# Performance work log

Measured on AMD Instinct MI355X. Metric: run time of the kernel, lower is better.

## Reference

```python
import jax, jax.numpy as jnp
import numpy as np

B, T, NIN, H, DMAX, K = 32, 128, 64, 512, 50, 4
D = DMAX + 1
TAU, THR, VRESET, REF_STEPS, DT, BETA = 10.0, 1.0, 0.0, 2, 1.0, 4.0


def setup_inputs() -> dict:
    key = jax.random.key(0)
    k0, k1, k2, k3 = jax.random.split(key, 4)
    spike_input = (jax.random.uniform(k0, (B, T, NIN)) < 0.05).astype(jnp.float32)
    w_ih = jax.random.normal(k1, (H, NIN)) * (1.0 / np.sqrt(NIN))
    delay_raw_ih = jax.random.normal(k2, (H, NIN))
    w_read = jax.random.normal(k3, (H,)) * (1.0 / np.sqrt(H))
    b_read = jnp.zeros((), jnp.float32)
    win = T // K
    mask = np.zeros((K, T), np.float32)
    for k in range(K):
        mask[k, k * win + 8:(k + 1) * win] = 1.0
    return {"spike_input": spike_input, "w_ih": w_ih, "delay_raw_ih": delay_raw_ih,
            "w_read": w_read, "b_read": b_read, "slot_mask": jnp.asarray(mask)}


@jax.custom_vjp
def spike_fn(x):
    return (x >= 0).astype(x.dtype)

def _sf_fwd(x):
    return spike_fn(x), x

def _sf_bwd(x, g):
    s = jax.nn.sigmoid(BETA * x)
    return (g * BETA * s * (1 - s),)

spike_fn.defvjp(_sf_fwd, _sf_bwd)


def reference(spike_input, w_ih, delay_raw_ih, w_read, b_read, slot_mask):
    # fractional per-synapse delays in [0, DMAX]
    d = jax.nn.sigmoid(delay_raw_ih) * DMAX        # [H, NIN]
    d0 = jnp.floor(d)
    frac = d - d0                                   # [H, NIN]
    i0 = d0.astype(jnp.int32)
    i1 = jnp.minimum(i0 + 1, DMAX)

    def gather(buf_t, idx):
        # buf_t [B, NIN, D], idx [H, NIN] -> [B, H, NIN]
        return jnp.take_along_axis(buf_t[:, None, :, :], idx[None, :, :, None], axis=-1)[..., 0]

    def step(carry, x_t):
        v, ref, buf, tot, fired = carry
        buf_t = jnp.swapaxes(buf, 1, 2)             # [B, NIN, D]
        delayed = gather(buf_t, i0) * (1 - frac) + gather(buf_t, i1) * frac  # [B,H,NIN]
        I = jnp.einsum('bhi,hi->bh', delayed, w_ih)
        not_ref = ref <= 0
        v_new = jnp.where(not_ref, v + (DT / TAU) * (-(v - VRESET) + I), v)
        spk = spike_fn(v_new - THR) * not_ref.astype(v.dtype)
        v_post = v_new * (1 - spk) + VRESET * spk
        ref_new = jnp.where(spk > 0, REF_STEPS, jnp.maximum(ref - 1, 0))
        # shift delay buffer: newest input at slot 0 (read happens BEFORE insert, as in source)
        buf_new = jnp.concatenate([x_t[:, None, :], buf[:, :-1, :]], axis=1)
        return (v_post, ref_new, buf_new, tot + spk.sum(1), jnp.maximum(fired, spk)), spk

    carry0 = (jnp.full((B, H), VRESET, jnp.float32),
              jnp.zeros((B, H), jnp.int32),
              jnp.zeros((B, D, NIN), jnp.float32),
              jnp.zeros((B,), jnp.float32),
              jnp.zeros((B, H), jnp.float32))
    xs = jnp.swapaxes(spike_input, 0, 1)            # [T, B, NIN]
    (_, _, _, total_h_spk, fired), spikes = jax.lax.scan(step, carry0, xs)
    # slot-windowed spike accumulation + linear readout
    acc = jnp.einsum('kt,tbh->bkh', slot_mask, spikes)
    logits = jnp.einsum('bkh,h->bk', acc, w_read) + b_read
    return logits
```

## Files before the change

### kernel.cpp

```cpp
#include <hip/hip_runtime.h>

#define NB 32
#define NT 128
#define NI 64
#define NH 512
#define HGB 32
#define PSTR 45
typedef unsigned long long u64;
typedef unsigned int u32;
typedef unsigned char u8;

#define OFF_P 0
#define OFF_BUF 23040
#define OFF_WL 23040
#define OFF_KL (23040 + 33280)
#define OFF_RL (OFF_KL + 2048)
#define OFF_MM (OFF_RL + 2048)
#define SMEM_BYTES (OFF_MM + 1024)

__global__ __launch_bounds__(1024, 4) void cur_kernel(
    const float* __restrict__ x, const float* __restrict__ w_ih,
    const float* __restrict__ draw, float4* __restrict__ Ig) {
  __shared__ char smem[SMEM_BYTES];
  u64* P = (u64*)(smem + OFF_P);
  float* xl = (float*)(smem + OFF_BUF);
  float4* Wl4 = (float4*)(smem + OFF_WL);
  u32* Klw = (u32*)(smem + OFF_KL);
  u32* Rlw = (u32*)(smem + OFF_RL);
  u64* Mm = (u64*)(smem + OFF_MM);

  const int tid = threadIdx.x;
  const int lane = tid & 63;
  const int wv = tid >> 6;
  const int hl = lane & 31;
  const int ch = lane >> 5;
  const int c = wv * 2 + ch;
  const int b = blockIdx.x;
  const int hg = blockIdx.y;

  {
    const float* xb = x + (size_t)b * (NT * NI);
    #pragma unroll
    for (int k2 = 0; k2 < 2; ++k2) {
      int e = (k2 * 1024 + tid) * 4;
      float4 v = *(const float4*)(xb + e);
      float* row = xl + (e >> 6) * (NI + 1) + (e & 63);
      row[0] = v.x; row[1] = v.y; row[2] = v.z; row[3] = v.w;
    }
  }
  __syncthreads();

  #pragma unroll
  for (int j = 0; j < 8; ++j) {
    int idx = wv * 8 + j;
    int i = idx >> 1;
    int h2 = idx & 1;
    u64 m = __ballot(xl[(h2 * 64 + lane) * (NI + 1) + i] != 0.0f);
    if (lane == 0) Mm[i * 2 + h2] = m;
  }
  __syncthreads();

  for (int idx = tid; idx < NI * PSTR; idx += 1024) {
    int i = idx / PSTR;
    int k = idx - i * PSTR;
    u64 m0 = Mm[i * 2], m1 = Mm[i * 2 + 1];
    u32 lo = 0, hi = 0;
    if (k >= 13) {
      int t = (k - 13) * 4;
      u32 nib = (u32)(((t < 64) ? (m0 >> t) : (m1 >> (t - 64))) & 15);
      lo = (nib * 0x00204081u) & 0x01010101u;
    }
    if (k + 1 >= 13 && k + 1 < 45) {
      int t = (k - 12) * 4;
      u32 nib = (u32)(((t < 64) ? (m0 >> t) : (m1 >> (t - 64))) & 15);
      hi = (nib * 0x00204081u) & 0x01010101u;
    }
    P[idx] = ((u64)hi << 32) | lo;
  }

  if (tid < 512) {
    int i4 = tid & 15, hh = tid >> 4;
    int h = hg * HGB + hh;
    float4 wv4 = *((const float4*)(w_ih + (size_t)h * NI) + i4);
    float4 rv4 = *((const float4*)(draw + (size_t)h * NI) + i4);
    float wa[4] = {wv4.x, wv4.y, wv4.z, wv4.w};
    float ra[4] = {rv4.x, rv4.y, rv4.z, rv4.w};
    float w0s[4], w1s[4];
    u32 kword = 0, rword = 0;
    #pragma unroll
    for (int jj = 0; jj < 4; ++jj) {
      float sig = 1.0f / (1.0f + expf(-ra[jj]));
      float d = sig * 50.0f;
      float d0f = floorf(d);
      float frac = d - d0f;
      int i0 = (int)d0f;
      float w0 = wa[jj] * (1.0f - frac);
      float w1 = wa[jj] * frac;
      if (i0 >= 50) { w0 += w1; w1 = 0.0f; i0 = 50; }
      w0s[jj] = w0; w1s[jj] = w1;
      int q = 50 - i0;
      kword |= (u32)(q >> 2) << (8 * jj);
      rword |= (u32)((q & 3) << 3) << (8 * jj);
    }
    Wl4[(2 * i4) * HGB + hh]     = make_float4(w0s[0], w1s[0], w0s[1], w1s[1]);
    Wl4[(2 * i4 + 1) * HGB + hh] = make_float4(w0s[2], w1s[2], w0s[3], w1s[3]);
    Klw[i4 * HGB + hh] = kword;
    Rlw[i4 * HGB + hh] = rword;
  }
  __syncthreads();

  float acc[4];
  #pragma unroll
  for (int j = 0; j < 4; ++j) acc[j] = 0.0f;

  u32 kall[16], rall[16];
  #pragma unroll
  for (int q = 0; q < 16; ++q) {
    kall[q] = Klw[q * HGB + hl];
    rall[q] = Rlw[q * HGB + hl];
  }
  const u64* Pc = P + c;

#define TAPS(IDX, W0, W1, KO, R8)                              \
  do {                                                         \
    u64 A = Pc[(IDX) * PSTR + (KO)];                           \
    u64 s1 = A >> (R8);                                        \
    u32 a0 = (u32)s1, a1 = (u32)(s1 >> 32);                    \
    float f0 = (float)(a0 & 255u);                             \
    float f1 = (float)((a0 >> 8) & 255u);                      \
    float f2 = (float)((a0 >> 16) & 255u);                     \
    float f3 = (float)(a0 >> 24);                              \
    float f4 = (float)(a1 & 255u);                             \
    acc[0] += (W0) * f1 + (W1) * f0;                           \
    acc[1] += (W0) * f2 + (W1) * f1;                           \
    acc[2] += (W0) * f3 + (W1) * f2;                           \
    acc[3] += (W0) * f4 + (W1) * f3;                           \
  } while (0)

  #pragma unroll
  for (int i4 = 0; i4 < 16; ++i4) {
    u32 kw = kall[i4];
    u32 rw = rall[i4];
    float4 wa = Wl4[(2 * i4) * HGB + hl];
    float4 wb = Wl4[(2 * i4 + 1) * HGB + hl];
    TAPS(4 * i4 + 0, wa.x, wa.y, (kw & 255u), (rw & 255u));
    TAPS(4 * i4 + 1, wa.z, wa.w, ((kw >> 8) & 255u), ((rw >> 8) & 255u));
    TAPS(4 * i4 + 2, wb.x, wb.y, ((kw >> 16) & 255u), ((rw >> 16) & 255u));
    TAPS(4 * i4 + 3, wb.z, wb.w, (kw >> 24), (rw >> 24));
    __builtin_amdgcn_sched_group_barrier(0x100, 2, 0);
    __builtin_amdgcn_sched_group_barrier(0x002, 26, 0);
    __builtin_amdgcn_sched_group_barrier(0x100, 2, 0);
    __builtin_amdgcn_sched_group_barrier(0x002, 26, 0);
    __builtin_amdgcn_sched_group_barrier(0x100, 2, 0);
    __builtin_amdgcn_sched_group_barrier(0x002, 26, 0);
  }
#undef TAPS

  Ig[((size_t)b * NH + hg * HGB + hl) * (NT / 4) + c] =
      make_float4(acc[0], acc[1], acc[2], acc[3]);
}

__global__ __launch_bounds__(512) void lifred_kernel(
    const float4* __restrict__ Ig, const float* __restrict__ w_read,
    const float* __restrict__ b_read, float* __restrict__ out) {
  const int b = blockIdx.x;
  const int tid = threadIdx.x;
  const float4* row = Ig + ((size_t)b * NH + tid) * (NT / 4);
  float v = 0.0f;
  int ref = 0;
  float c0 = 0.f, c1 = 0.f, c2 = 0.f, c3 = 0.f;
  float4 cur = row[0];
  #pragma unroll
  for (int gq = 0; gq < NT / 4; ++gq) {
    float4 nxt = (gq < NT / 4 - 1) ? row[gq + 1] : make_float4(0.f, 0.f, 0.f, 0.f);
    float Iv[4] = {cur.x, cur.y, cur.z, cur.w};
    #pragma unroll
    for (int j = 0; j < 4; ++j) {
      const int t = gq * 4 + j;
      float I = Iv[j];
      bool act = (ref <= 0);
      float vn = act ? (v + 0.1f * (I - v)) : v;
      bool spk = act && (vn >= 1.0f);
      v = spk ? 0.0f : vn;
      ref = spk ? 2 : (ref > 0 ? ref - 1 : 0);
      if ((t & 31) >= 8) {
        float inc = spk ? 1.0f : 0.0f;
        if (t < 32) c0 += inc;
        else if (t < 64) c1 += inc;
        else if (t < 96) c2 += inc;
        else c3 += inc;
      }
    }
    cur = nxt;
  }
  float wr = w_read[tid];
  float4 pv = make_float4(c0 * wr, c1 * wr, c2 * wr, c3 * wr);

  __shared__ float4 Pl[512];
  __shared__ float4 red[256];
  Pl[tid] = pv;
  __syncthreads();
  if (tid < 256) {
    float4 a = Pl[tid], d2 = Pl[tid + 256];
    red[tid] = make_float4(a.x + d2.x, a.y + d2.y, a.z + d2.z, a.w + d2.w);
  }
  __syncthreads();
  for (int off = 128; off > 0; off >>= 1) {
    if (tid < off) {
      float4 a = red[tid], d2 = red[tid + off];
      red[tid] = make_float4(a.x + d2.x, a.y + d2.y, a.z + d2.z, a.w + d2.w);
    }
    __syncthreads();
  }
  if (tid == 0) {
    float4 r = red[0];
    float br = b_read[0];
    out[b * 4 + 0] = r.x + br;
    out[b * 4 + 1] = r.y + br;
    out[b * 4 + 2] = r.z + br;
    out[b * 4 + 3] = r.w + br;
  }
}

extern "C" void kernel_launch(void* const* d_in, const int* in_sizes, int n_in,
                              void* d_out, int out_size, void* d_ws, size_t ws_size,
                              hipStream_t stream) {
  const float* x      = (const float*)d_in[0];
  const float* w_ih   = (const float*)d_in[1];
  const float* draw   = (const float*)d_in[2];
  const float* w_read = (const float*)d_in[3];
  const float* b_read = (const float*)d_in[4];

  char* ws = (char*)d_ws;
  float4* Ig  = (float4*)ws;
  float*  out = (float*)d_out;

  cur_kernel<<<dim3(NB, NH / HGB), dim3(1024), 0, stream>>>(
      x, w_ih, draw, Ig);
  lifred_kernel<<<dim3(NB), dim3(512), 0, stream>>>(
      Ig, w_read, b_read, out);
}
```

Measured before the change: 34.75 us.

## Transpose intermediate current layout, prefetch weights early, drop sched barriers

```diff
diff --git a/kernel.cpp b/kernel.cpp
--- a/kernel.cpp
+++ b/kernel.cpp
@@ -38,6 +38,15 @@
   const int b = blockIdx.x;
   const int hg = blockIdx.y;
 
+  float4 wv4h = make_float4(0.f, 0.f, 0.f, 0.f);
+  float4 rv4h = make_float4(0.f, 0.f, 0.f, 0.f);
+  if (tid < 512) {
+    int i4 = tid & 15, hh = tid >> 4;
+    int h = hg * HGB + hh;
+    wv4h = *((const float4*)(w_ih + (size_t)h * NI) + i4);
+    rv4h = *((const float4*)(draw + (size_t)h * NI) + i4);
+  }
+
   {
     const float* xb = x + (size_t)b * (NT * NI);
     #pragma unroll
@@ -80,11 +89,8 @@
 
   if (tid < 512) {
     int i4 = tid & 15, hh = tid >> 4;
-    int h = hg * HGB + hh;
-    float4 wv4 = *((const float4*)(w_ih + (size_t)h * NI) + i4);
-    float4 rv4 = *((const float4*)(draw + (size_t)h * NI) + i4);
-    float wa[4] = {wv4.x, wv4.y, wv4.z, wv4.w};
-    float ra[4] = {rv4.x, rv4.y, rv4.z, rv4.w};
+    float wa[4] = {wv4h.x, wv4h.y, wv4h.z, wv4h.w};
+    float ra[4] = {rv4h.x, rv4h.y, rv4h.z, rv4h.w};
     float w0s[4], w1s[4];
     u32 kword = 0, rword = 0;
     #pragma unroll
@@ -147,16 +153,10 @@
     TAPS(4 * i4 + 1, wa.z, wa.w, ((kw >> 8) & 255u), ((rw >> 8) & 255u));
     TAPS(4 * i4 + 2, wb.x, wb.y, ((kw >> 16) & 255u), ((rw >> 16) & 255u));
     TAPS(4 * i4 + 3, wb.z, wb.w, (kw >> 24), (rw >> 24));
-    __builtin_amdgcn_sched_group_barrier(0x100, 2, 0);
-    __builtin_amdgcn_sched_group_barrier(0x002, 26, 0);
-    __builtin_amdgcn_sched_group_barrier(0x100, 2, 0);
-    __builtin_amdgcn_sched_group_barrier(0x002, 26, 0);
-    __builtin_amdgcn_sched_group_barrier(0x100, 2, 0);
-    __builtin_amdgcn_sched_group_barrier(0x002, 26, 0);
   }
 #undef TAPS
 
-  Ig[((size_t)b * NH + hg * HGB + hl) * (NT / 4) + c] =
+  Ig[((size_t)c * NB + b) * NH + hg * HGB + hl] =
       make_float4(acc[0], acc[1], acc[2], acc[3]);
 }
 
@@ -165,14 +165,18 @@
     const float* __restrict__ b_read, float* __restrict__ out) {
   const int b = blockIdx.x;
   const int tid = threadIdx.x;
-  const float4* row = Ig + ((size_t)b * NH + tid) * (NT / 4);
+  const float wr = w_read[tid];
+  const float br = b_read[0];
+
   float v = 0.0f;
   int ref = 0;
   float c0 = 0.f, c1 = 0.f, c2 = 0.f, c3 = 0.f;
-  float4 cur = row[0];
+  float4 cur = Ig[(size_t)b * NH + tid];
   #pragma unroll
   for (int gq = 0; gq < NT / 4; ++gq) {
-    float4 nxt = (gq < NT / 4 - 1) ? row[gq + 1] : make_float4(0.f, 0.f, 0.f, 0.f);
+    float4 nxt = (gq < NT / 4 - 1)
+        ? Ig[((size_t)(gq + 1) * NB + b) * NH + tid]
+        : make_float4(0.f, 0.f, 0.f, 0.f);
     float Iv[4] = {cur.x, cur.y, cur.z, cur.w};
     #pragma unroll
     for (int j = 0; j < 4; ++j) {
@@ -193,7 +197,6 @@
     }
     cur = nxt;
   }
-  float wr = w_read[tid];
   float4 pv = make_float4(c0 * wr, c1 * wr, c2 * wr, c3 * wr);
 
   __shared__ float4 Pl[512];
@@ -214,7 +217,6 @@
   }
   if (tid == 0) {
     float4 r = red[0];
-    float br = b_read[0];
     out[b * 4 + 0] = r.x + br;
     out[b * 4 + 1] = r.y + br;
     out[b * 4 + 2] = r.z + br;
```

Result: faster. 30.82 us (-11.3%).
